# Optimization experiments

Hardware: AMD Instinct MI355X
Metric: run time of the kernel (lower is better)

## Reference

```python
import jax, jax.numpy as jnp
import numpy as np

TEMPERATURE = 0.75
SINKHORN_ITERS = 7
EPS = 1e-6
R_THRESH = 1e-3


def setup_inputs() -> dict:
    key = jax.random.key(0)
    k1, k2, k3, k4 = jax.random.split(key, 4)
    b, h, t, d = 1, 8, 2048, 64
    n = 32  # uniform buckets of size t // n = 64
    q = jax.random.normal(k1, (b, h, t, d), jnp.float32)
    k_ = jax.random.normal(k2, (b, h, t, d), jnp.float32)
    v = jax.random.normal(k3, (b, h, t, d), jnp.float32)
    gumbel_u = jax.random.uniform(k4, (b * h, n, n), jnp.float32)
    return {"q": q, "k": k_, "v": v, "gumbel_u": gumbel_u, "num_buckets": n}


def _sort_net_R(qm, km, gumbel_u, d):
    # qm, km: [bh, n, s, d] -> bucket sums [bh, n, d]
    q_sums = qm.sum(axis=2)
    k_sums = km.sum(axis=2)
    logits = jnp.einsum('bie,bje->bij', q_sums, k_sums) * (d ** -0.5)
    # gumbel_sinkhorn(relu(logits))
    r = jnp.log(jax.nn.relu(logits) + EPS)
    g = -jnp.log(-jnp.log(gumbel_u + EPS) + EPS)
    r = (r + g) / TEMPERATURE
    for _ in range(SINKHORN_ITERS):
        r = r - jax.nn.logsumexp(r, axis=2, keepdims=True)
        r = r - jax.nn.logsumexp(r, axis=1, keepdims=True)
    return jnp.exp(r)  # [bh, n, n]


def reference(q, k, v, gumbel_u, num_buckets):
    b, h, t, d = q.shape
    bh = b * h
    n = num_buckets
    s = t // n  # uniform bucket size
    qm = q.reshape(bh, n, s, d)
    km = k.reshape(bh, n, s, d)
    vm = v.reshape(bh, n, s, d)

    R = _sort_net_R(qm, km, gumbel_u, d)
    # torch skips pairs with R_ij <= 1e-3 (output is zero); multiply by masked R
    Rm = jnp.where(R > R_THRESH, R, 0.0)

    scale = d ** -0.5
    # keys for pair (i, j) are concat(k_i, k_j): split score into self + cross
    S_self = jnp.einsum('bise,bite->bist', qm, km) * scale          # [bh,n,s,s]
    S_cross = jnp.einsum('bise,bjte->bijst', qm, km) * scale        # [bh,n,n,s,s]
    scores = jnp.concatenate(
        [jnp.broadcast_to(S_self[:, :, None], (bh, n, n, s, s)), S_cross],
        axis=-1)                                                    # [bh,n,n,s,2s]
    w = jax.nn.softmax(scores, axis=-1)
    w_i, w_j = w[..., :s], w[..., s:]
    # out_ij = (w_i @ v_i + w_j @ v_j) * R_ij, summed over j
    out = (jnp.einsum('bijst,bite,bij->bise', w_i, vm, Rm)
           + jnp.einsum('bijst,bjte,bij->bise', w_j, vm, Rm))       # [bh,n,s,d]
    return out.reshape(b, h, t, d)
```

## Files before the change

### kernel.cpp

```cpp
#include <hip/hip_runtime.h>
#include <math.h>
#include <stdint.h>

#define BH 8
#define NB 32
#define SS 64
#define DD 64
#define TT 2048

typedef float f32x16 __attribute__((ext_vector_type(16)));
typedef short bf16x8 __attribute__((ext_vector_type(8)));
typedef unsigned short u16;

__device__ __forceinline__ unsigned pkbf(float a, float b) {
  unsigned r;
  asm("v_cvt_pk_bf16_f32 %0, %1, %2" : "=v"(r) : "v"(a), "v"(b));
  return r;
}
__device__ __forceinline__ float exp2x(float x) {
  float r;
  asm("v_exp_f32 %0, %1" : "=v"(r) : "v"(x));
  return r;
}
__device__ __forceinline__ float log2x(float x) {
  float r;
  asm("v_log_f32 %0, %1" : "=v"(r) : "v"(x));
  return r;
}
__device__ __forceinline__ bf16x8 pack8v(const f32x16& v, const int b) {
  union { unsigned u[4]; bf16x8 v8; } x;
  x.u[0] = pkbf(v[b + 0], v[b + 1]);
  x.u[1] = pkbf(v[b + 2], v[b + 3]);
  x.u[2] = pkbf(v[b + 4], v[b + 5]);
  x.u[3] = pkbf(v[b + 6], v[b + 7]);
  return x.v8;
}

__global__ __launch_bounds__(256) void prep_kernel(
    const float* __restrict__ q, const float* __restrict__ k, const float* __restrict__ v,
    u16* __restrict__ qb, u16* __restrict__ kb, u16* __restrict__ vtb,
    float* __restrict__ qsum, float* __restrict__ ksum)
{
  __shared__ float qt[64][68];
  __shared__ float kt[64][68];
  __shared__ float vt[64][68];

  const int T = blockIdx.x;
  const int t = threadIdx.x;
  const float* qsrc = q + (size_t)T * 4096;
  const float* ksrc = k + (size_t)T * 4096;
  const float* vsrc = v + (size_t)T * 4096;

#pragma unroll
  for (int r4 = 0; r4 < 4; ++r4) {
    int f = r4 * 256 + t;
    int row = f >> 4, c4 = (f & 15) << 2;
    *(float4*)&qt[row][c4] = ((const float4*)qsrc)[f];
    *(float4*)&kt[row][c4] = ((const float4*)ksrc)[f];
    *(float4*)&vt[row][c4] = ((const float4*)vsrc)[f];
  }
  __syncthreads();

  const float qscale = 0.18033688011112042f;

#pragma unroll
  for (int half = 0; half < 2; ++half) {
    int x = half * 256 + t;
    int c = x >> 6, lane = x & 63;
    int l31 = lane & 31, hi = lane >> 5;
    int m = c >> 2, s = c & 3;
    int row = l31 + 32 * m;
    int cb = 16 * s + 4 * hi;
    float4 a = *(const float4*)&qt[row][cb];
    float4 b = *(const float4*)&qt[row][cb + 8];
    uint4 o;
    o.x = pkbf(a.x * qscale, a.y * qscale);
    o.y = pkbf(a.z * qscale, a.w * qscale);
    o.z = pkbf(b.x * qscale, b.y * qscale);
    o.w = pkbf(b.z * qscale, b.w * qscale);
    *(uint4*)(qb + (size_t)T * 4096 + (size_t)x * 8) = o;

    float4 ka = *(const float4*)&kt[row][cb];
    float4 kb4 = *(const float4*)&kt[row][cb + 8];
    uint4 ko;
    ko.x = pkbf(ka.x, ka.y);
    ko.y = pkbf(ka.z, ka.w);
    ko.z = pkbf(kb4.x, kb4.y);
    ko.w = pkbf(kb4.z, kb4.w);
    *(uint4*)(kb + (size_t)T * 4096 + (size_t)x * 8) = ko;

    int d = l31 + 32 * m;
    int kb0 = 16 * s + 4 * hi;
    uint4 vo;
    vo.x = pkbf(vt[kb0 + 0][d], vt[kb0 + 1][d]);
    vo.y = pkbf(vt[kb0 + 2][d], vt[kb0 + 3][d]);
    vo.z = pkbf(vt[kb0 + 8][d], vt[kb0 + 9][d]);
    vo.w = pkbf(vt[kb0 + 10][d], vt[kb0 + 11][d]);
    *(uint4*)(vtb + (size_t)T * 4096 + (size_t)x * 8) = vo;
  }

  if (t < 64) {
    float s = 0.f;
#pragma unroll 8
    for (int r = 0; r < 64; ++r) s += qt[r][t];
    qsum[T * 64 + t] = s;
  } else if (t < 128) {
    int c = t - 64;
    float s = 0.f;
#pragma unroll 8
    for (int r = 0; r < 64; ++r) s += kt[r][c];
    ksum[T * 64 + c] = s;
  }
}

__global__ __launch_bounds__(256, 1) void sink_kernel(
    const float* __restrict__ qsum, const float* __restrict__ ksum,
    const float* __restrict__ gu, float* __restrict__ Rm)
{
  __shared__ float qs[32 * 65];
  __shared__ float ks[32 * 65];
  __shared__ float LT[32 * 33];

  const int bh = blockIdx.x;
  const int t = threadIdx.x;
  const float L2E = 1.4426950408889634f;
  const float LN2 = 0.6931471805599453f;

  {
    int idx = t * 8;
    float4 a = *(const float4*)(qsum + bh * 2048 + idx);
    float4 b = *(const float4*)(qsum + bh * 2048 + idx + 4);
    float4 c = *(const float4*)(ksum + bh * 2048 + idx);
    float4 d = *(const float4*)(ksum + bh * 2048 + idx + 4);
    int bkt = idx >> 6, e = idx & 63;
    float* qd = qs + bkt * 65 + e;
    qd[0] = a.x; qd[1] = a.y; qd[2] = a.z; qd[3] = a.w;
    qd[4] = b.x; qd[5] = b.y; qd[6] = b.z; qd[7] = b.w;
    float* kd = ks + bkt * 65 + e;
    kd[0] = c.x; kd[1] = c.y; kd[2] = c.z; kd[3] = c.w;
    kd[4] = d.x; kd[5] = d.y; kd[6] = d.z; kd[7] = d.w;
  }
  __syncthreads();

  {
    const int i0 = t >> 5, j = t & 31;
#pragma unroll
    for (int x = 0; x < 4; ++x) {
      int ii = i0 + 8 * x;
      float acc = 0.f;
      for (int e = 0; e < 64; ++e) acc += qs[ii * 65 + e] * ks[j * 65 + e];
      acc *= 0.125f;
      float u = gu[bh * 1024 + ii * 32 + j];
      float gg = -logf(-logf(u + 1e-6f) + 1e-6f);
      LT[ii * 33 + j] = (logf(fmaxf(acc, 0.f) + 1e-6f) + gg) * (1.0f / 0.75f);
    }
  }
  __syncthreads();

  if (t < 64) {
    const int l = t;
    const int half16 = (l & 1) * 16;
    const int major = l >> 1;
    float r[16];
#pragma unroll
    for (int x = 0; x < 16; ++x) r[x] = LT[major * 33 + half16 + x];

    for (int it = 0; it < 7; ++it) {
      {
        float e[16];
#pragma unroll
        for (int x = 0; x < 16; ++x) e[x] = exp2x(r[x] * L2E);
#pragma unroll
        for (int off = 8; off > 0; off >>= 1)
#pragma unroll
          for (int x = 0; x < off; ++x) e[x] += e[x + off];
        float s = e[0] + __shfl_xor(e[0], 1, 64);
        float L = log2x(fmaxf(s, 1e-30f)) * LN2;
#pragma unroll
        for (int x = 0; x < 16; ++x) r[x] -= L;
      }
#pragma unroll
      for (int x = 0; x < 16; ++x) LT[major * 33 + half16 + x] = r[x];
#pragma unroll
      for (int x = 0; x < 16; ++x) r[x] = LT[(half16 + x) * 33 + major];
      {
        float e[16];
#pragma unroll
        for (int x = 0; x < 16; ++x) e[x] = exp2x(r[x] * L2E);
#pragma unroll
        for (int off = 8; off > 0; off >>= 1)
#pragma unroll
          for (int x = 0; x < off; ++x) e[x] += e[x + off];
        float s = e[0] + __shfl_xor(e[0], 1, 64);
        float L = log2x(fmaxf(s, 1e-30f)) * LN2;
#pragma unroll
        for (int x = 0; x < 16; ++x) r[x] -= L;
      }
      if (it < 6) {
#pragma unroll
        for (int x = 0; x < 16; ++x) LT[(half16 + x) * 33 + major] = r[x];
#pragma unroll
        for (int x = 0; x < 16; ++x) r[x] = LT[major * 33 + half16 + x];
      }
    }

#pragma unroll
    for (int x = 0; x < 16; ++x) {
      float R = exp2x(r[x] * L2E);
      LT[(half16 + x) * 33 + major] = (R > 1e-3f) ? R : 0.f;
    }
  }
  __syncthreads();

  {
    int idx = t * 4;
    int i0 = idx >> 5, j0 = idx & 31;
    float4 o;
    o.x = LT[i0 * 33 + j0 + 0];
    o.y = LT[i0 * 33 + j0 + 1];
    o.z = LT[i0 * 33 + j0 + 2];
    o.w = LT[i0 * 33 + j0 + 3];
    *(float4*)(Rm + bh * 1024 + idx) = o;
  }
}

__global__ __launch_bounds__(512) void attn_kernel(
    const u16* __restrict__ qb, const u16* __restrict__ kb,
    const u16* __restrict__ vtb, const float* __restrict__ Rm,
    float* __restrict__ out)
{
  __shared__ __align__(16) unsigned char smem[35840];
  float (*redh)[2][32][68] = (float (*)[2][32][68])smem;
  float (*cbuf)[32] = (float (*)[32])(smem + 34816);

  const int bh  = blockIdx.x & 7;
  const int i   = blockIdx.x >> 3;
  const int t   = threadIdx.x;
  const int w   = t >> 6;
  const int n   = w & 1;
  const int g   = w >> 1;
  const int lane = t & 63;
  const int l31 = lane & 31;
  const int hi  = lane >> 5;

  const u16* qtile = qb + ((size_t)(bh * NB + i)) * 4096;
  const u16* kbh   = kb + (size_t)bh * NB * 4096;
  const u16* vbh   = vtb + (size_t)bh * NB * 4096;

#define LOADG(dst, base)                                                      \
  {                                                                           \
    _Pragma("unroll") for (int m = 0; m < 2; ++m)                             \
    _Pragma("unroll") for (int s = 0; s < 4; ++s)                             \
      dst[m][s] = *(const bf16x8*)((base) + ((size_t)((m * 4 + s) * 64 + lane)) * 8); \
  }

  float rij8[8];
#pragma unroll
  for (int jj = 0; jj < 8; ++jj) rij8[jj] = Rm[bh * 1024 + i * 32 + g + 4 * jj];

  bf16x8 qB[4];
#pragma unroll
  for (int s = 0; s < 4; ++s)
    qB[s] = *(const bf16x8*)(qtile + ((size_t)((n * 4 + s) * 64 + lane)) * 8);

  bf16x8 kA[2][4], vB[2][4];
  LOADG(kA, kbh + (size_t)g * 4096);
  LOADG(vB, vbh + (size_t)g * 4096);

  float m0, S0;
  bf16x8 psA[4];
  {
    const u16* kib = kbh + (size_t)i * 4096;
    bf16x8 kAi[2][4];
    LOADG(kAi, kib);
    f32x16 aS0, aS1;
#pragma unroll
    for (int r = 0; r < 16; ++r) { aS0[r] = 0.f; aS1[r] = 0.f; }
#pragma unroll
    for (int s = 0; s < 4; ++s) {
      aS0 = __builtin_amdgcn_mfma_f32_32x32x16_bf16(kAi[0][s], qB[s], aS0, 0, 0, 0);
      aS1 = __builtin_amdgcn_mfma_f32_32x32x16_bf16(kAi[1][s], qB[s], aS1, 0, 0, 0);
    }
    float mx[16];
#pragma unroll
    for (int r = 0; r < 16; ++r) mx[r] = fmaxf(aS0[r], aS1[r]);
#pragma unroll
    for (int off = 8; off > 0; off >>= 1)
#pragma unroll
      for (int r = 0; r < off; ++r) mx[r] = fmaxf(mx[r], mx[r + off]);
    float mm = fmaxf(mx[0], __shfl_xor(mx[0], 32, 64));
#pragma unroll
    for (int r = 0; r < 16; ++r) { aS0[r] = exp2x(aS0[r] - mm); aS1[r] = exp2x(aS1[r] - mm); }
    float sm[16];
#pragma unroll
    for (int r = 0; r < 16; ++r) sm[r] = aS0[r] + aS1[r];
#pragma unroll
    for (int off = 8; off > 0; off >>= 1)
#pragma unroll
      for (int r = 0; r < off; ++r) sm[r] += sm[r + off];
    S0 = sm[0] + __shfl_xor(sm[0], 32, 64);
    m0 = mm;
    psA[0] = pack8v(aS0, 0);
    psA[1] = pack8v(aS0, 8);
    psA[2] = pack8v(aS1, 0);
    psA[3] = pack8v(aS1, 8);
  }

  f32x16 outAcc[2];
#pragma unroll
  for (int nv = 0; nv < 2; ++nv)
#pragma unroll
    for (int e = 0; e < 16; ++e) outAcc[nv][e] = 0.f;
  float cacc = 0.f;

#pragma unroll
  for (int jj = 0; jj < 8; ++jj) {
    const int j = g + 4 * jj;
    const float rij = rij8[jj];

    f32x16 a0, a1;
#pragma unroll
    for (int r = 0; r < 16; ++r) { a0[r] = 0.f; a1[r] = 0.f; }
    __builtin_amdgcn_s_setprio(1);
#pragma unroll
    for (int s = 0; s < 4; ++s) {
      a0 = __builtin_amdgcn_mfma_f32_32x32x16_bf16(kA[0][s], qB[s], a0, 0, 0, 0);
      a1 = __builtin_amdgcn_mfma_f32_32x32x16_bf16(kA[1][s], qB[s], a1, 0, 0, 0);
    }
    __builtin_amdgcn_s_setprio(0);

    if (jj < 7) LOADG(kA, kbh + (size_t)(j + 4) * 4096);

    float mx[16];
#pragma unroll
    for (int r = 0; r < 16; ++r) mx[r] = fmaxf(a0[r], a1[r]);
#pragma unroll
    for (int off = 8; off > 0; off >>= 1)
#pragma unroll
      for (int r = 0; r < off; ++r) mx[r] = fmaxf(mx[r], mx[r + off]);
    float mc = fmaxf(mx[0], __shfl_xor(mx[0], 32, 64));
    float mj = fmaxf(m0, mc);
#pragma unroll
    for (int r = 0; r < 16; ++r) { a0[r] = exp2x(a0[r] - mj); a1[r] = exp2x(a1[r] - mj); }
    float sm[16];
#pragma unroll
    for (int r = 0; r < 16; ++r) sm[r] = a0[r] + a1[r];
#pragma unroll
    for (int off = 8; off > 0; off >>= 1)
#pragma unroll
      for (int r = 0; r < off; ++r) sm[r] += sm[r + off];
    float ssum = sm[0] + __shfl_xor(sm[0], 32, 64);
    float e0 = exp2x(m0 - mj);
    float den = S0 * e0 + ssum;
    float inv = rij / den;
    cacc += e0 * inv;
#pragma unroll
    for (int r = 0; r < 16; ++r) { a0[r] *= inv; a1[r] *= inv; }

    __builtin_amdgcn_s_setprio(1);
#pragma unroll
    for (int s = 0; s < 4; ++s) {
      bf16x8 wf = (s < 2) ? pack8v(a0, 8 * (s & 1)) : pack8v(a1, 8 * (s & 1));
      outAcc[0] = __builtin_amdgcn_mfma_f32_32x32x16_bf16(wf, vB[0][s], outAcc[0], 0, 0, 0);
      outAcc[1] = __builtin_amdgcn_mfma_f32_32x32x16_bf16(wf, vB[1][s], outAcc[1], 0, 0, 0);
    }
    __builtin_amdgcn_s_setprio(0);

    if (jj < 7) LOADG(vB, vbh + (size_t)(j + 4) * 4096);
  }

  {
    const u16* vib = vbh + (size_t)i * 4096;
    bf16x8 vBi[2][4];
    LOADG(vBi, vib);
    f32x16 U[2];
#pragma unroll
    for (int nv = 0; nv < 2; ++nv)
#pragma unroll
      for (int e = 0; e < 16; ++e) U[nv][e] = 0.f;
#pragma unroll
    for (int s = 0; s < 4; ++s) {
      U[0] = __builtin_amdgcn_mfma_f32_32x32x16_bf16(psA[s], vBi[0][s], U[0], 0, 0, 0);
      U[1] = __builtin_amdgcn_mfma_f32_32x32x16_bf16(psA[s], vBi[1][s], U[1], 0, 0, 0);
    }
    if (hi == 0) cbuf[w][l31] = cacc;
    __syncthreads();
#pragma unroll
    for (int r = 0; r < 16; ++r) {
      int row = (r & 3) + 8 * (r >> 2) + 4 * hi;
      float cr = cbuf[w][row];
      outAcc[0][r] += U[0][r] * cr;
      outAcc[1][r] += U[1][r] * cr;
    }
  }

#define RED_W(buf)                                                         \
  {                                                                        \
    _Pragma("unroll") for (int ne = 0; ne < 2; ++ne)                       \
    _Pragma("unroll") for (int r = 0; r < 16; ++r) {                       \
      int row = (r & 3) + 8 * (r >> 2) + 4 * hi;                           \
      (buf)[row][l31 + 32 * ne] = outAcc[ne][r];                           \
    }                                                                      \
  }
#define RED_A(buf)                                                         \
  {                                                                        \
    _Pragma("unroll") for (int ne = 0; ne < 2; ++ne)                       \
    _Pragma("unroll") for (int r = 0; r < 16; ++r) {                       \
      int row = (r & 3) + 8 * (r >> 2) + 4 * hi;                           \
      outAcc[ne][r] += (buf)[row][l31 + 32 * ne];                          \
    }                                                                      \
  }

  if (g >= 2) RED_W(redh[n][g - 2]);
  __syncthreads();
  if (g < 2) RED_A(redh[n][g]);
  __syncthreads();
  if (g == 1) RED_W(redh[n][0]);
  __syncthreads();
  if (g == 0) {
    RED_A(redh[n][0]);
    RED_W(redh[n][0]);
  }
  __syncthreads();

  {
    int row = t >> 3;
    int nr = row >> 5, lrow = row & 31;
    int col0 = (t & 7) * 8;
    float4 a = *(const float4*)&redh[nr][0][lrow][col0];
    float4 b = *(const float4*)&redh[nr][0][lrow][col0 + 4];
    float* ob = out + ((size_t)bh * TT + i * SS + row) * DD + col0;
    *(float4*)ob = a;
    *(float4*)(ob + 4) = b;
  }
#undef LOADG
#undef RED_W
#undef RED_A
}

extern "C" void kernel_launch(void* const* d_in, const int* in_sizes, int n_in,
                              void* d_out, int out_size, void* d_ws, size_t ws_size,
                              hipStream_t stream) {
  (void)in_sizes; (void)n_in; (void)out_size; (void)ws_size;
  const float* q  = (const float*)d_in[0];
  const float* k  = (const float*)d_in[1];
  const float* v  = (const float*)d_in[2];
  const float* gu = (const float*)d_in[3];
  float* out = (float*)d_out;

  char* wsb = (char*)d_ws;
  u16* qb   = (u16*)(wsb);
  u16* kb   = (u16*)(wsb + (1 << 21));
  u16* vtb  = (u16*)(wsb + (2 << 21));
  float* qsum = (float*)(wsb + (3 << 21));
  float* ksum = (float*)(wsb + (3 << 21) + (1 << 16));
  float* Rm   = (float*)(wsb + (3 << 21) + (2 << 16));

  prep_kernel<<<256, 256, 0, stream>>>(q, k, v, qb, kb, vtb, qsum, ksum);
  sink_kernel<<<BH, 256, 0, stream>>>(qsum, ksum, gu, Rm);
  attn_kernel<<<BH * NB, 512, 0, stream>>>(qb, kb, vtb, Rm, out);
}
```

Measured before the change: 35.52 us.

## Fuse sinkhorn kernel into prep kernel via last-block atomic counter

Removes the separate sinkhorn launch by having the last prep block per head, detected with an atomic counter and threadfences, run the sinkhorn normalization, reusing the prep kernel's shared memory. This is meant to remove one kernel launch and the launch gap between prep and sinkhorn. In exchange it adds a memset launch to reset the counters, plus atomics and fences on every block. The sinkhorn work now runs at the tail of prep on only 8 blocks.

```diff
diff --git a/kernel.cpp b/kernel.cpp
--- a/kernel.cpp
+++ b/kernel.cpp
@@ -38,12 +38,15 @@
 
 __global__ __launch_bounds__(256) void prep_kernel(
     const float* __restrict__ q, const float* __restrict__ k, const float* __restrict__ v,
+    const float* __restrict__ gu,
     u16* __restrict__ qb, u16* __restrict__ kb, u16* __restrict__ vtb,
-    float* __restrict__ qsum, float* __restrict__ ksum)
+    float* __restrict__ qsum, float* __restrict__ ksum,
+    float* __restrict__ Rm, unsigned* __restrict__ cnt)
 {
   __shared__ float qt[64][68];
   __shared__ float kt[64][68];
   __shared__ float vt[64][68];
+  __shared__ int lastFlag;
 
   const int T = blockIdx.x;
   const int t = threadIdx.x;
@@ -111,20 +114,23 @@
     for (int r = 0; r < 64; ++r) s += kt[r][c];
     ksum[T * 64 + c] = s;
   }
-}
-
-__global__ __launch_bounds__(256, 1) void sink_kernel(
-    const float* __restrict__ qsum, const float* __restrict__ ksum,
-    const float* __restrict__ gu, float* __restrict__ Rm)
-{
-  __shared__ float qs[32 * 65];
-  __shared__ float ks[32 * 65];
-  __shared__ float LT[32 * 33];
-
-  const int bh = blockIdx.x;
-  const int t = threadIdx.x;
+
+  __syncthreads();
+  if (t == 0) {
+    __threadfence();
+    unsigned old = atomicAdd(&cnt[T >> 5], 1u);
+    lastFlag = (old == 31u);
+  }
+  __syncthreads();
+  if (!lastFlag) return;
+  __threadfence();
+
+  const int bh = T >> 5;
   const float L2E = 1.4426950408889634f;
   const float LN2 = 0.6931471805599453f;
+  float* qs = &qt[0][0];
+  float* ks = qs + 32 * 65;
+  float* LT = ks + 32 * 65;
 
   {
     int idx = t * 8;
@@ -455,8 +461,9 @@
   float* qsum = (float*)(wsb + (3 << 21));
   float* ksum = (float*)(wsb + (3 << 21) + (1 << 16));
   float* Rm   = (float*)(wsb + (3 << 21) + (2 << 16));
-
-  prep_kernel<<<256, 256, 0, stream>>>(q, k, v, qb, kb, vtb, qsum, ksum);
-  sink_kernel<<<BH, 256, 0, stream>>>(qsum, ksum, gu, Rm);
+  unsigned* cnt = (unsigned*)(wsb + (3 << 21) + (3 << 16));
+
+  hipMemsetAsync(cnt, 0, BH * sizeof(unsigned), stream);
+  prep_kernel<<<256, 256, 0, stream>>>(q, k, v, gu, qb, kb, vtb, qsum, ksum, Rm, cnt);
   attn_kernel<<<BH * NB, 512, 0, stream>>>(qb, kb, vtb, Rm, out);
 }
```

Result: slower. 45.93 us (+29.3%).

## Fuse Sinkhorn computation into attention kernel, recomputing per block

Applied to the files above, without the earlier changes.

Removes the separate sink_kernel launch and has every attention block recompute the full 32x32 Sinkhorn matrix for its head in shared memory, then read its own row of R. This drops one kernel launch and the serial dependency on an 8-block kernel. In exchange, the Sinkhorn work is repeated 32 times per head, and each attention block now runs a serial prologue with several barriers before its MFMA work starts. Global loads for K/V tiles are issued before the prologue so they can overlap it.

```diff
diff --git a/kernel.cpp b/kernel.cpp
--- a/kernel.cpp
+++ b/kernel.cpp
@@ -113,125 +113,18 @@
   }
 }
 
-__global__ __launch_bounds__(256, 1) void sink_kernel(
-    const float* __restrict__ qsum, const float* __restrict__ ksum,
-    const float* __restrict__ gu, float* __restrict__ Rm)
-{
-  __shared__ float qs[32 * 65];
-  __shared__ float ks[32 * 65];
-  __shared__ float LT[32 * 33];
-
-  const int bh = blockIdx.x;
-  const int t = threadIdx.x;
-  const float L2E = 1.4426950408889634f;
-  const float LN2 = 0.6931471805599453f;
-
-  {
-    int idx = t * 8;
-    float4 a = *(const float4*)(qsum + bh * 2048 + idx);
-    float4 b = *(const float4*)(qsum + bh * 2048 + idx + 4);
-    float4 c = *(const float4*)(ksum + bh * 2048 + idx);
-    float4 d = *(const float4*)(ksum + bh * 2048 + idx + 4);
-    int bkt = idx >> 6, e = idx & 63;
-    float* qd = qs + bkt * 65 + e;
-    qd[0] = a.x; qd[1] = a.y; qd[2] = a.z; qd[3] = a.w;
-    qd[4] = b.x; qd[5] = b.y; qd[6] = b.z; qd[7] = b.w;
-    float* kd = ks + bkt * 65 + e;
-    kd[0] = c.x; kd[1] = c.y; kd[2] = c.z; kd[3] = c.w;
-    kd[4] = d.x; kd[5] = d.y; kd[6] = d.z; kd[7] = d.w;
-  }
-  __syncthreads();
-
-  {
-    const int i0 = t >> 5, j = t & 31;
-#pragma unroll
-    for (int x = 0; x < 4; ++x) {
-      int ii = i0 + 8 * x;
-      float acc = 0.f;
-      for (int e = 0; e < 64; ++e) acc += qs[ii * 65 + e] * ks[j * 65 + e];
-      acc *= 0.125f;
-      float u = gu[bh * 1024 + ii * 32 + j];
-      float gg = -logf(-logf(u + 1e-6f) + 1e-6f);
-      LT[ii * 33 + j] = (logf(fmaxf(acc, 0.f) + 1e-6f) + gg) * (1.0f / 0.75f);
-    }
-  }
-  __syncthreads();
-
-  if (t < 64) {
-    const int l = t;
-    const int half16 = (l & 1) * 16;
-    const int major = l >> 1;
-    float r[16];
-#pragma unroll
-    for (int x = 0; x < 16; ++x) r[x] = LT[major * 33 + half16 + x];
-
-    for (int it = 0; it < 7; ++it) {
-      {
-        float e[16];
-#pragma unroll
-        for (int x = 0; x < 16; ++x) e[x] = exp2x(r[x] * L2E);
-#pragma unroll
-        for (int off = 8; off > 0; off >>= 1)
-#pragma unroll
-          for (int x = 0; x < off; ++x) e[x] += e[x + off];
-        float s = e[0] + __shfl_xor(e[0], 1, 64);
-        float L = log2x(fmaxf(s, 1e-30f)) * LN2;
-#pragma unroll
-        for (int x = 0; x < 16; ++x) r[x] -= L;
-      }
-#pragma unroll
-      for (int x = 0; x < 16; ++x) LT[major * 33 + half16 + x] = r[x];
-#pragma unroll
-      for (int x = 0; x < 16; ++x) r[x] = LT[(half16 + x) * 33 + major];
-      {
-        float e[16];
-#pragma unroll
-        for (int x = 0; x < 16; ++x) e[x] = exp2x(r[x] * L2E);
-#pragma unroll
-        for (int off = 8; off > 0; off >>= 1)
-#pragma unroll
-          for (int x = 0; x < off; ++x) e[x] += e[x + off];
-        float s = e[0] + __shfl_xor(e[0], 1, 64);
-        float L = log2x(fmaxf(s, 1e-30f)) * LN2;
-#pragma unroll
-        for (int x = 0; x < 16; ++x) r[x] -= L;
-      }
-      if (it < 6) {
-#pragma unroll
-        for (int x = 0; x < 16; ++x) LT[(half16 + x) * 33 + major] = r[x];
-#pragma unroll
-        for (int x = 0; x < 16; ++x) r[x] = LT[major * 33 + half16 + x];
-      }
-    }
-
-#pragma unroll
-    for (int x = 0; x < 16; ++x) {
-      float R = exp2x(r[x] * L2E);
-      LT[(half16 + x) * 33 + major] = (R > 1e-3f) ? R : 0.f;
-    }
-  }
-  __syncthreads();
-
-  {
-    int idx = t * 4;
-    int i0 = idx >> 5, j0 = idx & 31;
-    float4 o;
-    o.x = LT[i0 * 33 + j0 + 0];
-    o.y = LT[i0 * 33 + j0 + 1];
-    o.z = LT[i0 * 33 + j0 + 2];
-    o.w = LT[i0 * 33 + j0 + 3];
-    *(float4*)(Rm + bh * 1024 + idx) = o;
-  }
-}
-
 __global__ __launch_bounds__(512) void attn_kernel(
     const u16* __restrict__ qb, const u16* __restrict__ kb,
-    const u16* __restrict__ vtb, const float* __restrict__ Rm,
+    const u16* __restrict__ vtb, const float* __restrict__ qsum,
+    const float* __restrict__ ksum, const float* __restrict__ gu,
     float* __restrict__ out)
 {
   __shared__ __align__(16) unsigned char smem[35840];
   float (*redh)[2][32][68] = (float (*)[2][32][68])smem;
   float (*cbuf)[32] = (float (*)[32])(smem + 34816);
+  float* qs = (float*)smem;
+  float* ks = qs + 32 * 65;
+  float* LT = ks + 32 * 65;
 
   const int bh  = blockIdx.x & 7;
   const int i   = blockIdx.x >> 3;
@@ -254,25 +147,113 @@
       dst[m][s] = *(const bf16x8*)((base) + ((size_t)((m * 4 + s) * 64 + lane)) * 8); \
   }
 
-  float rij8[8];
-#pragma unroll
-  for (int jj = 0; jj < 8; ++jj) rij8[jj] = Rm[bh * 1024 + i * 32 + g + 4 * jj];
-
   bf16x8 qB[4];
 #pragma unroll
   for (int s = 0; s < 4; ++s)
     qB[s] = *(const bf16x8*)(qtile + ((size_t)((n * 4 + s) * 64 + lane)) * 8);
-
-  bf16x8 kA[2][4], vB[2][4];
+  bf16x8 kA[2][4], vB[2][4], kAi[2][4];
   LOADG(kA, kbh + (size_t)g * 4096);
   LOADG(vB, vbh + (size_t)g * 4096);
+  LOADG(kAi, kbh + (size_t)i * 4096);
+
+  float rij8[8];
+  {
+    const float L2E = 1.4426950408889634f;
+    const float LN2 = 0.6931471805599453f;
+
+    if (t < 256) {
+      int idx = t * 8;
+      float4 a = *(const float4*)(qsum + bh * 2048 + idx);
+      float4 b = *(const float4*)(qsum + bh * 2048 + idx + 4);
+      float4 c = *(const float4*)(ksum + bh * 2048 + idx);
+      float4 d = *(const float4*)(ksum + bh * 2048 + idx + 4);
+      int bkt = idx >> 6, e = idx & 63;
+      float* qd = qs + bkt * 65 + e;
+      qd[0] = a.x; qd[1] = a.y; qd[2] = a.z; qd[3] = a.w;
+      qd[4] = b.x; qd[5] = b.y; qd[6] = b.z; qd[7] = b.w;
+      float* kd = ks + bkt * 65 + e;
+      kd[0] = c.x; kd[1] = c.y; kd[2] = c.z; kd[3] = c.w;
+      kd[4] = d.x; kd[5] = d.y; kd[6] = d.z; kd[7] = d.w;
+    }
+    __syncthreads();
+
+    if (t < 256) {
+      const int i0 = t >> 5, j = t & 31;
+#pragma unroll
+      for (int x = 0; x < 4; ++x) {
+        int ii = i0 + 8 * x;
+        float acc = 0.f;
+        for (int e = 0; e < 64; ++e) acc += qs[ii * 65 + e] * ks[j * 65 + e];
+        acc *= 0.125f;
+        float u = gu[bh * 1024 + ii * 32 + j];
+        float gg = -logf(-logf(u + 1e-6f) + 1e-6f);
+        LT[ii * 33 + j] = (logf(fmaxf(acc, 0.f) + 1e-6f) + gg) * (1.0f / 0.75f);
+      }
+    }
+    __syncthreads();
+
+    if (t < 64) {
+      const int l = t;
+      const int half16 = (l & 1) * 16;
+      const int major = l >> 1;
+      float r[16];
+#pragma unroll
+      for (int x = 0; x < 16; ++x) r[x] = LT[major * 33 + half16 + x];
+
+      for (int it = 0; it < 7; ++it) {
+        {
+          float e[16];
+#pragma unroll
+          for (int x = 0; x < 16; ++x) e[x] = exp2x(r[x] * L2E);
+#pragma unroll
+          for (int off = 8; off > 0; off >>= 1)
+#pragma unroll
+            for (int x = 0; x < off; ++x) e[x] += e[x + off];
+          float s = e[0] + __shfl_xor(e[0], 1, 64);
+          float L = log2x(fmaxf(s, 1e-30f)) * LN2;
+#pragma unroll
+          for (int x = 0; x < 16; ++x) r[x] -= L;
+        }
+#pragma unroll
+        for (int x = 0; x < 16; ++x) LT[major * 33 + half16 + x] = r[x];
+#pragma unroll
+        for (int x = 0; x < 16; ++x) r[x] = LT[(half16 + x) * 33 + major];
+        {
+          float e[16];
+#pragma unroll
+          for (int x = 0; x < 16; ++x) e[x] = exp2x(r[x] * L2E);
+#pragma unroll
+          for (int off = 8; off > 0; off >>= 1)
+#pragma unroll
+            for (int x = 0; x < off; ++x) e[x] += e[x + off];
+          float s = e[0] + __shfl_xor(e[0], 1, 64);
+          float L = log2x(fmaxf(s, 1e-30f)) * LN2;
+#pragma unroll
+          for (int x = 0; x < 16; ++x) r[x] -= L;
+        }
+        if (it < 6) {
+#pragma unroll
+          for (int x = 0; x < 16; ++x) LT[(half16 + x) * 33 + major] = r[x];
+#pragma unroll
+          for (int x = 0; x < 16; ++x) r[x] = LT[major * 33 + half16 + x];
+        }
+      }
+
+#pragma unroll
+      for (int x = 0; x < 16; ++x) {
+        float R = exp2x(r[x] * L2E);
+        LT[(half16 + x) * 33 + major] = (R > 1e-3f) ? R : 0.f;
+      }
+    }
+    __syncthreads();
+
+#pragma unroll
+    for (int jj = 0; jj < 8; ++jj) rij8[jj] = LT[i * 33 + g + 4 * jj];
+  }
 
   float m0, S0;
   bf16x8 psA[4];
   {
-    const u16* kib = kbh + (size_t)i * 4096;
-    bf16x8 kAi[2][4];
-    LOADG(kAi, kib);
     f32x16 aS0, aS1;
 #pragma unroll
     for (int r = 0; r < 16; ++r) { aS0[r] = 0.f; aS1[r] = 0.f; }
@@ -454,9 +435,7 @@
   u16* vtb  = (u16*)(wsb + (2 << 21));
   float* qsum = (float*)(wsb + (3 << 21));
   float* ksum = (float*)(wsb + (3 << 21) + (1 << 16));
-  float* Rm   = (float*)(wsb + (3 << 21) + (2 << 16));
 
   prep_kernel<<<256, 256, 0, stream>>>(q, k, v, qb, kb, vtb, qsum, ksum);
-  sink_kernel<<<BH, 256, 0, stream>>>(qsum, ksum, gu, Rm);
-  attn_kernel<<<BH * NB, 512, 0, stream>>>(qb, kb, vtb, Rm, out);
-}
+  attn_kernel<<<BH * NB, 512, 0, stream>>>(qb, kb, vtb, qsum, ksum, gu, out);
+}
```

After: 34.22 us. 1.04x faster.
